# Optimization experiments

Hardware: AMD Instinct MI355X
Metric: run time of the kernel (lower is better)

Reference implementation:

```python
import jax, jax.numpy as jnp
import numpy as np


def setup_inputs() -> dict:
    key = jax.random.key(0)
    k_u, k_a, k_b, k_c, k_d = jax.random.split(key, 5)
    n_dim, m_dim, p_dim = 1024, 1024, 1024
    batch, T = 8, 2048
    u = jax.random.normal(k_u, (batch, T, m_dim), dtype=jnp.float32)
    A = jax.random.normal(k_a, (n_dim, n_dim), dtype=jnp.float32) / np.sqrt(n_dim).astype(np.float32)
    B = jax.random.normal(k_b, (n_dim, m_dim), dtype=jnp.float32)
    C = jax.random.normal(k_c, (p_dim, n_dim), dtype=jnp.float32)
    D = jax.random.normal(k_d, (p_dim, m_dim), dtype=jnp.float32)
    return {"u": u, "A": A, "B": B, "C": C, "D": D}


def reference(u, A, B, C, D):
    # NOTE: torch.einsum('bn,nn->bn', x, A.T) with repeated label 'n' on the
    # second operand takes the DIAGONAL of A. So the recurrence is
    #   x_k = x_{k-1} * diag(A) + u_k @ B^T
    #   y_k = x_k @ C^T + u_k @ D^T
    a = jnp.diagonal(A)  # (n,)
    # Precompute time-invariant input projection in one big GEMM: (b, T, n)
    Bu = jnp.einsum('btm,nm->btn', u, B)
    batch = u.shape[0]
    x0 = jnp.zeros((batch, a.shape[0]), dtype=u.dtype)

    def step(x, bu_k):
        x = x * a + bu_k
        return x, x

    # scan over time: Bu transposed to (T, b, n)
    _, X = jax.lax.scan(step, x0, jnp.swapaxes(Bu, 0, 1))
    X = jnp.swapaxes(X, 0, 1)  # (b, T, n)
    y = jnp.einsum('btn,pn->btp', X, C) + jnp.einsum('btm,pm->btp', u, D)
    return y
```

## Files before the change

kernel.cpp:

```cpp
#include <hip/hip_runtime.h>
#include <hip/hip_bf16.h>
#include <stdint.h>


typedef __attribute__((ext_vector_type(8))) short short8;
typedef __attribute__((ext_vector_type(4))) float floatx4;

#define BM 128
#define BN 128
#define BK 32

__device__ __forceinline__ uint16_t f2bf(float f) {
    union { float f; uint32_t u; } v; v.f = f;
    uint32_t u = v.u;
    return (uint16_t)((u + 0x7FFFu + ((u >> 16) & 1u)) >> 16);
}

__device__ __forceinline__ uint32_t pk_bf16(float x, float y) {
    union { __hip_bfloat162 h; uint32_t u; } v;
    v.h = __float22bfloat162_rn(make_float2(x, y));
    return v.u;
}

__device__ __forceinline__ float bf2f(uint16_t b) {
    union { uint32_t u; float f; } v; v.u = ((uint32_t)b) << 16;
    return v.f;
}

__global__ void cvt_all(const float* __restrict__ u, const float* __restrict__ B,
                        const float* __restrict__ C, const float* __restrict__ D,
                        uint16_t* __restrict__ u_bf, uint16_t* __restrict__ B_bf,
                        uint16_t* __restrict__ C_bf, uint16_t* __restrict__ D_bf,
                        unsigned* __restrict__ counter, int n4u, int n4w) {
    int i = blockIdx.x * blockDim.x + threadIdx.x;
    if (i == 0) *counter = 0u;
    const float* src; uint16_t* dst; int idx;
    if (i < n4u)                { src = u; dst = u_bf; idx = i; }
    else if (i < n4u + n4w)     { src = B; dst = B_bf; idx = i - n4u; }
    else if (i < n4u + 2 * n4w) { src = C; dst = C_bf; idx = i - n4u - n4w; }
    else if (i < n4u + 3 * n4w) { src = D; dst = D_bf; idx = i - n4u - 2 * n4w; }
    else return;
    float4 v = ((const float4*)src)[idx];
    uint2 o;
    o.x = pk_bf16(v.x, v.y);
    o.y = pk_bf16(v.z, v.w);
    ((uint2*)dst)[idx] = o;
}

#define CHUNK 128
#define LOOKBACK 64
__global__ void scan_kernel(const uint16_t* __restrict__ Bu, const float* __restrict__ Amat,
                            uint16_t* __restrict__ Xbf, int T, int Nn) {
    int n2 = blockIdx.z * blockDim.x + threadIdx.x;
    int n = n2 * 2;
    int b = blockIdx.y;
    int chunk = blockIdx.x;
    float a0 = Amat[(size_t)n * Nn + n];
    float a1 = Amat[(size_t)(n + 1) * Nn + n + 1];
    const uint32_t* bu = (const uint32_t*)(Bu + ((size_t)b * T) * Nn) + n2;
    uint32_t* xp = (uint32_t*)(Xbf + ((size_t)b * T) * Nn) + n2;
    const int halfN = Nn >> 1;
    int t0 = chunk * CHUNK;
    int ts = t0 - LOOKBACK; if (ts < 0) ts = 0;
    float x0 = 0.f, x1 = 0.f;
    for (int t = ts; t < t0; ++t) {
        uint32_t w = bu[(size_t)t * halfN];
        x0 = x0 * a0 + bf2f((uint16_t)w);
        x1 = x1 * a1 + bf2f((uint16_t)(w >> 16));
    }
    for (int t = t0; t < t0 + CHUNK; ++t) {
        uint32_t w = bu[(size_t)t * halfN];
        x0 = x0 * a0 + bf2f((uint16_t)w);
        x1 = x1 * a1 + bf2f((uint16_t)(w >> 16));
        xp[(size_t)t * halfN] = pk_bf16(x0, x1);
    }
}

template <bool OUT_BF16, bool ARRIVE>
__global__ void gemm_bt(const uint16_t* __restrict__ A0, const uint16_t* __restrict__ W0,
                        const uint16_t* __restrict__ A1, const uint16_t* __restrict__ W1,
                        void* __restrict__ Cout, int M, int N, int K, int nseg,
                        unsigned* counter) {
    __shared__ alignas(16) uint16_t As[BM * BK];
    __shared__ alignas(16) uint16_t Bs[BN * BK];

    const int tid  = threadIdx.x;
    const int wave = tid >> 6;
    const int lane = tid & 63;
    const int quad = lane >> 4;
    const int l16  = lane & 15;
    const int bx   = blockIdx.x;
    const int by   = blockIdx.y;
    const int m0 = bx * BM;
    const int n0 = by * BN;
    const int wr = (wave >> 1) * 64;
    const int wc = (wave & 1) * 64;

    floatx4 acc[4][4];
#pragma unroll
    for (int i = 0; i < 4; ++i)
#pragma unroll
        for (int j = 0; j < 4; ++j) acc[i][j] = (floatx4)(0.f);

    for (int seg = 0; seg < nseg; ++seg) {
        const uint16_t* A = seg ? A1 : A0;
        const uint16_t* W = seg ? W1 : W0;
        for (int k0 = 0; k0 < K; k0 += BK) {
            __syncthreads();
#pragma unroll
            for (int r = 0; r < 2; ++r) {
                int L = r * 256 + tid;
                int row = L >> 2;
                int col = (L & 3) * 8;
                const uint16_t* gp = A + (size_t)(m0 + row) * K + k0 + col;
                uint16_t* lb = &As[(size_t)(r * 256 + wave * 64) * 8];
                __builtin_amdgcn_global_load_lds(
                    (const __attribute__((address_space(1))) void*)gp,
                    (__attribute__((address_space(3))) void*)lb, 16, 0, 0);
            }
#pragma unroll
            for (int r = 0; r < 2; ++r) {
                int L = r * 256 + tid;
                int row = L >> 2;
                int col = (L & 3) * 8;
                const uint16_t* gp = W + (size_t)(n0 + row) * K + k0 + col;
                uint16_t* lb = &Bs[(size_t)(r * 256 + wave * 64) * 8];
                __builtin_amdgcn_global_load_lds(
                    (const __attribute__((address_space(1))) void*)gp,
                    (__attribute__((address_space(3))) void*)lb, 16, 0, 0);
            }
            __syncthreads();

            short8 af[4], bf[4];
#pragma unroll
            for (int i = 0; i < 4; ++i)
                af[i] = *(const short8*)&As[(wr + i * 16 + l16) * BK + quad * 8];
#pragma unroll
            for (int j = 0; j < 4; ++j)
                bf[j] = *(const short8*)&Bs[(wc + j * 16 + l16) * BK + quad * 8];
#pragma unroll
            for (int i = 0; i < 4; ++i)
#pragma unroll
                for (int j = 0; j < 4; ++j)
                    acc[i][j] = __builtin_amdgcn_mfma_f32_16x16x32_bf16(
                        af[i], bf[j], acc[i][j], 0, 0, 0);
        }
    }

    if (ARRIVE) {
        __syncthreads();
        const int nbx = (int)gridDim.x;
        const unsigned total = gridDim.x * gridDim.y;
        bool spinner = (bx >= nbx - 8) || (bx == nbx - 9 && by == 7);
        if (tid == 0) {
            __threadfence();
            __hip_atomic_fetch_add(counter, 1u, __ATOMIC_RELEASE,
                                   __HIP_MEMORY_SCOPE_AGENT);
            if (spinner) {
                while (__hip_atomic_load(counter, __ATOMIC_ACQUIRE,
                                         __HIP_MEMORY_SCOPE_AGENT) < total) {
                    __builtin_amdgcn_s_sleep(32);
                }
            }
        }
        if (spinner) __syncthreads();
    }

#pragma unroll
    for (int i = 0; i < 4; ++i)
#pragma unroll
        for (int j = 0; j < 4; ++j)
#pragma unroll
            for (int r = 0; r < 4; ++r) {
                int row = m0 + wr + i * 16 + quad * 4 + r;
                int col = n0 + wc + j * 16 + l16;
                if (OUT_BF16)
                    ((uint16_t*)Cout)[(size_t)row * N + col] = f2bf(acc[i][j][r]);
                else
                    ((float*)Cout)[(size_t)row * N + col] = acc[i][j][r];
            }
}

extern "C" void kernel_launch(void* const* d_in, const int* in_sizes, int n_in,
                              void* d_out, int out_size, void* d_ws, size_t ws_size,
                              hipStream_t stream) {
    const float* u = (const float*)d_in[0];
    const float* A = (const float*)d_in[1];
    const float* B = (const float*)d_in[2];
    const float* C = (const float*)d_in[3];
    const float* D = (const float*)d_in[4];
    float* y = (float*)d_out;

    const int batch = 8, T = 2048, Kd = 1024, Nd = 1024;
    const int M = batch * T;
    const size_t MB = 1024 * 1024;

    uint16_t* u_bf = (uint16_t*)d_ws;
    uint16_t* X_bf = u_bf + (size_t)M * Kd;
    uint16_t* B_bf = X_bf;
    uint16_t* Bu_bf = (uint16_t*)d_out;

    const int n4u = (M * Kd) / 4;
    const int n4w = (Nd * Kd) / 4;
    const dim3 ggrid(M / BM, Nd / BN);

    if (ws_size >= 68 * MB) {
        uint16_t* C_bf = X_bf + (size_t)M * Nd;
        uint16_t* D_bf = C_bf + (size_t)Nd * Kd;
        unsigned* counter = (unsigned*)((char*)d_out + 60 * MB - 4);

        cvt_all<<<(n4u + 3 * n4w) / 256, 256, 0, stream>>>(
            u, B, C, D, u_bf, B_bf, C_bf, D_bf, counter, n4u, n4w);
        gemm_bt<true, false><<<ggrid, 256, 0, stream>>>(
            u_bf, B_bf, nullptr, nullptr, Bu_bf, M, Nd, Kd, 1, nullptr);
        scan_kernel<<<dim3(T / CHUNK, batch, Nd / 512), 256, 0, stream>>>(
            Bu_bf, A, X_bf, T, Nd);
        gemm_bt<false, false><<<ggrid, 256, 0, stream>>>(
            X_bf, C_bf, u_bf, D_bf, y, M, Nd, Kd, 2, nullptr);
    } else {
        uint16_t* C_bf = (uint16_t*)((char*)d_out + 60 * MB);
        uint16_t* D_bf = (uint16_t*)((char*)d_out + 62 * MB);
        unsigned* counter = (unsigned*)((char*)d_out + 60 * MB - 4);

        cvt_all<<<(n4u + 3 * n4w) / 256, 256, 0, stream>>>(
            u, B, C, D, u_bf, B_bf, C_bf, D_bf, counter, n4u, n4w);
        gemm_bt<true, false><<<ggrid, 256, 0, stream>>>(
            u_bf, B_bf, nullptr, nullptr, Bu_bf, M, Nd, Kd, 1, nullptr);
        scan_kernel<<<dim3(T / CHUNK, batch, Nd / 512), 256, 0, stream>>>(
            Bu_bf, A, X_bf, T, Nd);
        gemm_bt<false, true><<<ggrid, 256, 0, stream>>>(
            X_bf, C_bf, u_bf, D_bf, y, M, Nd, Kd, 2, counter);
    }
}
```

Measured before the change: 274.5 us.

## Rewrite GEMM as 256x256 tile, double-buffered LDS pipeline with swizzle

Replaces the 128x128x32 single-buffered GEMM with a 256x256 tile, BK=64, 512-thread kernel. It double-buffers LDS through async global_load_lds staging interleaved with four MFMA phases, adds an XOR swizzle against LDS bank conflicts, and raises wave priority around MFMA blocks. The aim is to hide global-load latency, raise arithmetic intensity and cut barrier overhead per FLOP. The cost is heavier LDS use (128KB per block) and register pressure, fewer blocks on the grid, and fragile manual vmcnt accounting. The spinner condition for the grid barrier is adjusted to the new grid shape.

```diff
diff --git a/kernel.cpp b/kernel.cpp
--- a/kernel.cpp
+++ b/kernel.cpp
@@ -5,10 +5,6 @@
 
 typedef __attribute__((ext_vector_type(8))) short short8;
 typedef __attribute__((ext_vector_type(4))) float floatx4;
-
-#define BM 128
-#define BN 128
-#define BK 32
 
 __device__ __forceinline__ uint16_t f2bf(float f) {
     union { float f; uint32_t u; } v; v.f = f;
@@ -76,82 +72,149 @@
     }
 }
 
+
+#define BARRIER_F() do { asm volatile("" ::: "memory"); \
+    __builtin_amdgcn_s_barrier(); \
+    asm volatile("" ::: "memory"); } while (0)
+
+#define MIDSYNC() do { BARRIER_F(); \
+    asm volatile("s_waitcnt lgkmcnt(0)" ::: "memory"); \
+    __builtin_amdgcn_sched_barrier(0); } while (0)
+
 template <bool OUT_BF16, bool ARRIVE>
-__global__ void gemm_bt(const uint16_t* __restrict__ A0, const uint16_t* __restrict__ W0,
-                        const uint16_t* __restrict__ A1, const uint16_t* __restrict__ W1,
-                        void* __restrict__ Cout, int M, int N, int K, int nseg,
-                        unsigned* counter) {
-    __shared__ alignas(16) uint16_t As[BM * BK];
-    __shared__ alignas(16) uint16_t Bs[BN * BK];
+__global__ __launch_bounds__(512, 2)
+void gemm_bt(const uint16_t* __restrict__ A0, const uint16_t* __restrict__ W0,
+             const uint16_t* __restrict__ A1, const uint16_t* __restrict__ W1,
+             void* __restrict__ Cout, int M, int N, int K, int nseg,
+             unsigned* counter) {
+    __shared__ alignas(16) uint16_t As[2][256 * 64];
+    __shared__ alignas(16) uint16_t Bs[2][256 * 64];
 
     const int tid  = threadIdx.x;
     const int wave = tid >> 6;
     const int lane = tid & 63;
     const int quad = lane >> 4;
     const int l16  = lane & 15;
-    const int bx   = blockIdx.x;
-    const int by   = blockIdx.y;
-    const int m0 = bx * BM;
-    const int n0 = by * BN;
-    const int wr = (wave >> 1) * 64;
-    const int wc = (wave & 1) * 64;
-
-    floatx4 acc[4][4];
-#pragma unroll
-    for (int i = 0; i < 4; ++i)
+    const int wr   = wave >> 2;
+    const int wc   = wave & 3;
+    const int bx = blockIdx.x, by = blockIdx.y;
+    const int m0 = bx * 256;
+    const int n0 = by * 256;
+    const int NT = nseg << 4;
+
+    const int srow = tid >> 3;
+    const int sgc2 = ((tid & 7) << 4) ^ ((srow & 7) << 4);
+    const size_t rowbytes = (size_t)(2 * K);
+
+    auto stage = [&](int e) {
+        int tau = e >> 2;
+        if (tau >= NT) return;
+        int half = e & 3;
+        int seg  = tau >> 4;
+        int k0b  = (tau & 15) << 7;
+        const uint16_t* G; char* L; int row0, rh;
+        if (half < 2) { G = seg ? W1 : W0; L = (char*)Bs + ((tau & 1) << 15); row0 = n0; rh = half; }
+        else          { G = seg ? A1 : A0; L = (char*)As + ((tau & 1) << 15); row0 = m0; rh = half - 2; }
+        const char* gb = (const char*)G + (size_t)(row0 + rh * 128 + srow) * rowbytes + k0b + sgc2;
+        char* lb = L + rh * 16384 + wave * 1024;
+#pragma unroll
+        for (int c = 0; c < 2; ++c) {
+            __builtin_amdgcn_global_load_lds(
+                (const __attribute__((address_space(1))) void*)(gb + (size_t)c * 64 * rowbytes),
+                (__attribute__((address_space(3))) void*)(lb + c * 8192), 16, 0, 0);
+        }
+    };
+
+    const int swz  = l16 & 7;
+    const int arow = wr * 128 + l16;
+    const int brow = wc * 64 + l16;
+
+#define LDA8(i, s) (*(const short8*)(Ab + (size_t)((arow + (i) * 16) * 128) + (((((s) << 2) | quad) ^ swz) << 4)))
+#define LDB8(j, s) (*(const short8*)(Bb + (size_t)((brow + (j) * 16) * 128) + (((((s) << 2) | quad) ^ swz) << 4)))
+
+    floatx4 acc[8][4];
+#pragma unroll
+    for (int i = 0; i < 8; ++i)
 #pragma unroll
         for (int j = 0; j < 4; ++j) acc[i][j] = (floatx4)(0.f);
 
-    for (int seg = 0; seg < nseg; ++seg) {
-        const uint16_t* A = seg ? A1 : A0;
-        const uint16_t* W = seg ? W1 : W0;
-        for (int k0 = 0; k0 < K; k0 += BK) {
-            __syncthreads();
-#pragma unroll
-            for (int r = 0; r < 2; ++r) {
-                int L = r * 256 + tid;
-                int row = L >> 2;
-                int col = (L & 3) * 8;
-                const uint16_t* gp = A + (size_t)(m0 + row) * K + k0 + col;
-                uint16_t* lb = &As[(size_t)(r * 256 + wave * 64) * 8];
-                __builtin_amdgcn_global_load_lds(
-                    (const __attribute__((address_space(1))) void*)gp,
-                    (__attribute__((address_space(3))) void*)lb, 16, 0, 0);
-            }
-#pragma unroll
-            for (int r = 0; r < 2; ++r) {
-                int L = r * 256 + tid;
-                int row = L >> 2;
-                int col = (L & 3) * 8;
-                const uint16_t* gp = W + (size_t)(n0 + row) * K + k0 + col;
-                uint16_t* lb = &Bs[(size_t)(r * 256 + wave * 64) * 8];
-                __builtin_amdgcn_global_load_lds(
-                    (const __attribute__((address_space(1))) void*)gp,
-                    (__attribute__((address_space(3))) void*)lb, 16, 0, 0);
-            }
-            __syncthreads();
-
-            short8 af[4], bf[4];
-#pragma unroll
-            for (int i = 0; i < 4; ++i)
-                af[i] = *(const short8*)&As[(wr + i * 16 + l16) * BK + quad * 8];
-#pragma unroll
-            for (int j = 0; j < 4; ++j)
-                bf[j] = *(const short8*)&Bs[(wc + j * 16 + l16) * BK + quad * 8];
-#pragma unroll
-            for (int i = 0; i < 4; ++i)
-#pragma unroll
-                for (int j = 0; j < 4; ++j)
-                    acc[i][j] = __builtin_amdgcn_mfma_f32_16x16x32_bf16(
-                        af[i], bf[j], acc[i][j], 0, 0, 0);
+#pragma unroll
+    for (int e = 0; e < 7; ++e) stage(e);
+    asm volatile("s_waitcnt vmcnt(6)" ::: "memory");
+    __builtin_amdgcn_sched_barrier(0);
+    BARRIER_F();
+
+    for (int t = 0; t < NT; ++t) {
+        const char* Ab = (const char*)As + ((t & 1) << 15);
+        const char* Bb = (const char*)Bs + ((t & 1) << 15);
+
+        short8 b0[4], b1[4], aA[4];
+#pragma unroll
+        for (int j = 0; j < 4; ++j) { b0[j] = LDB8(j, 0); b1[j] = LDB8(j, 1); }
+#pragma unroll
+        for (int i = 0; i < 4; ++i) aA[i] = LDA8(i, 0);
+        stage(4 * t + 7);
+        MIDSYNC();
+        __builtin_amdgcn_s_setprio(1);
+#pragma unroll
+        for (int i = 0; i < 4; ++i)
+#pragma unroll
+            for (int j = 0; j < 4; ++j)
+                acc[i][j] = __builtin_amdgcn_mfma_f32_16x16x32_bf16(aA[i], b0[j], acc[i][j], 0, 0, 0);
+        __builtin_amdgcn_s_setprio(0);
+        BARRIER_F();
+
+        short8 aB[4];
+#pragma unroll
+        for (int i = 0; i < 4; ++i) aB[i] = LDA8(i, 1);
+        stage(4 * t + 8);
+        MIDSYNC();
+        __builtin_amdgcn_s_setprio(1);
+#pragma unroll
+        for (int i = 0; i < 4; ++i)
+#pragma unroll
+            for (int j = 0; j < 4; ++j)
+                acc[i][j] = __builtin_amdgcn_mfma_f32_16x16x32_bf16(aB[i], b1[j], acc[i][j], 0, 0, 0);
+        __builtin_amdgcn_s_setprio(0);
+        BARRIER_F();
+
+        short8 aC[4], aD[4];
+#pragma unroll
+        for (int i = 0; i < 4; ++i) { aC[i] = LDA8(4 + i, 0); aD[i] = LDA8(4 + i, 1); }
+        stage(4 * t + 9);
+        MIDSYNC();
+        __builtin_amdgcn_s_setprio(1);
+#pragma unroll
+        for (int i = 0; i < 4; ++i)
+#pragma unroll
+            for (int j = 0; j < 4; ++j)
+                acc[4 + i][j] = __builtin_amdgcn_mfma_f32_16x16x32_bf16(aC[i], b0[j], acc[4 + i][j], 0, 0, 0);
+        __builtin_amdgcn_s_setprio(0);
+        BARRIER_F();
+
+        stage(4 * t + 10);
+        BARRIER_F();
+        __builtin_amdgcn_s_setprio(1);
+#pragma unroll
+        for (int i = 0; i < 4; ++i)
+#pragma unroll
+            for (int j = 0; j < 4; ++j)
+                acc[4 + i][j] = __builtin_amdgcn_mfma_f32_16x16x32_bf16(aD[i], b1[j], acc[4 + i][j], 0, 0, 0);
+        __builtin_amdgcn_s_setprio(0);
+        if (t + 2 < NT) {
+            asm volatile("s_waitcnt vmcnt(6)" ::: "memory");
+        } else if (t + 1 < NT) {
+            asm volatile("s_waitcnt vmcnt(0)" ::: "memory");
         }
+        __builtin_amdgcn_sched_barrier(0);
+        BARRIER_F();
     }
 
     if (ARRIVE) {
         __syncthreads();
         const int nbx = (int)gridDim.x;
         const unsigned total = gridDim.x * gridDim.y;
-        bool spinner = (bx >= nbx - 8) || (bx == nbx - 9 && by == 7);
+        bool spinner = (bx >= nbx - 4) || (bx == nbx - 5 && by == (int)gridDim.y - 1);
         if (tid == 0) {
             __threadfence();
             __hip_atomic_fetch_add(counter, 1u, __ATOMIC_RELEASE,
@@ -167,18 +230,20 @@
     }
 
 #pragma unroll
-    for (int i = 0; i < 4; ++i)
+    for (int i = 0; i < 8; ++i)
 #pragma unroll
         for (int j = 0; j < 4; ++j)
 #pragma unroll
             for (int r = 0; r < 4; ++r) {
-                int row = m0 + wr + i * 16 + quad * 4 + r;
-                int col = n0 + wc + j * 16 + l16;
+                int row = m0 + wr * 128 + i * 16 + quad * 4 + r;
+                int col = n0 + wc * 64 + j * 16 + l16;
                 if (OUT_BF16)
                     ((uint16_t*)Cout)[(size_t)row * N + col] = f2bf(acc[i][j][r]);
                 else
                     ((float*)Cout)[(size_t)row * N + col] = acc[i][j][r];
             }
+#undef LDA8
+#undef LDB8
 }
 
 extern "C" void kernel_launch(void* const* d_in, const int* in_sizes, int n_in,
@@ -202,7 +267,7 @@
 
     const int n4u = (M * Kd) / 4;
     const int n4w = (Nd * Kd) / 4;
-    const dim3 ggrid(M / BM, Nd / BN);
+    const dim3 ggrid(M / 256, Nd / 256);
 
     if (ws_size >= 68 * MB) {
         uint16_t* C_bf = X_bf + (size_t)M * Nd;
@@ -211,11 +276,11 @@
 
         cvt_all<<<(n4u + 3 * n4w) / 256, 256, 0, stream>>>(
             u, B, C, D, u_bf, B_bf, C_bf, D_bf, counter, n4u, n4w);
-        gemm_bt<true, false><<<ggrid, 256, 0, stream>>>(
+        gemm_bt<true, false><<<ggrid, 512, 0, stream>>>(
             u_bf, B_bf, nullptr, nullptr, Bu_bf, M, Nd, Kd, 1, nullptr);
         scan_kernel<<<dim3(T / CHUNK, batch, Nd / 512), 256, 0, stream>>>(
             Bu_bf, A, X_bf, T, Nd);
-        gemm_bt<false, false><<<ggrid, 256, 0, stream>>>(
+        gemm_bt<false, false><<<ggrid, 512, 0, stream>>>(
             X_bf, C_bf, u_bf, D_bf, y, M, Nd, Kd, 2, nullptr);
     } else {
         uint16_t* C_bf = (uint16_t*)((char*)d_out + 60 * MB);
@@ -224,11 +289,11 @@
 
         cvt_all<<<(n4u + 3 * n4w) / 256, 256, 0, stream>>>(
             u, B, C, D, u_bf, B_bf, C_bf, D_bf, counter, n4u, n4w);
-        gemm_bt<true, false><<<ggrid, 256, 0, stream>>>(
+        gemm_bt<true, false><<<ggrid, 512, 0, stream>>>(
             u_bf, B_bf, nullptr, nullptr, Bu_bf, M, Nd, Kd, 1, nullptr);
         scan_kernel<<<dim3(T / CHUNK, batch, Nd / 512), 256, 0, stream>>>(
             Bu_bf, A, X_bf, T, Nd);
-        gemm_bt<false, true><<<ggrid, 256, 0, stream>>>(
+        gemm_bt<false, true><<<ggrid, 512, 0, stream>>>(
             X_bf, C_bf, u_bf, D_bf, y, M, Nd, Kd, 2, counter);
     }
 }
```

New measurement: 262.3 us. 4.5% less time.
